# Performance work log

Hardware: AMD Instinct MI355X
Metric: run time of the kernel (lower is better)

## Reference

```python
import jax, jax.numpy as jnp
import numpy as np

N, E = 50000, 800000
IN_DIM, OUT_DIM, EDGE_DIM = 128, 128, 6
LN_EPS = 1e-5


def setup_inputs() -> dict:
    key = jax.random.key(0)
    ks = jax.random.split(key, 9)
    w = lambda k, sh: (jax.random.normal(k, sh, jnp.float32) * 0.05)
    return {
        "x": jax.random.normal(ks[0], (N, IN_DIM), jnp.float32),
        "edge_attr": jax.random.normal(ks[1], (E, EDGE_DIM), jnp.float32),
        "Wn": w(ks[2], (IN_DIM, OUT_DIM)),
        "bn": jnp.zeros((OUT_DIM,), jnp.float32),
        "We": w(ks[3], (EDGE_DIM, OUT_DIM)),
        "be": jnp.zeros((OUT_DIM,), jnp.float32),
        "Wm": w(ks[4], (2 * OUT_DIM, OUT_DIM)),
        "bm": jnp.zeros((OUT_DIM,), jnp.float32),
        "gamma": jnp.ones((OUT_DIM,), jnp.float32),
        "beta": jnp.zeros((OUT_DIM,), jnp.float32),
        "edge_index": jax.random.randint(ks[5], (2, E), 0, N, jnp.int32),
    }


def reference(x, edge_attr, Wn, bn, We, be, Wm, bm, gamma, beta, edge_index):
    row, col = edge_index[0], edge_index[1]
    x_t = x @ Wn + bn                                  # [N, D]
    e_t = edge_attr @ We + be                          # [E, D]
    msgs = jnp.concatenate([x_t[col], e_t], axis=-1)   # gather + concat [E, 2D]
    msgs = jax.nn.relu(msgs @ Wm + bm)                 # [E, D]
    agg = jax.ops.segment_sum(msgs, row, num_segments=N)            # scatter_add
    deg = jax.ops.segment_sum(jnp.ones((E,), jnp.float32), row, num_segments=N)
    out = agg / jnp.clip(deg, 1.0)[:, None] + x_t      # mean-normalize + residual
    mu = out.mean(axis=-1, keepdims=True)
    var = out.var(axis=-1, keepdims=True)
    return (out - mu) * jax.lax.rsqrt(var + LN_EPS) * gamma + beta
```

## Files before the change

kernel.cpp:

```cpp
#include <hip/hip_runtime.h>
#include <hip/hip_bf16.h>

#define D 128
#define EDGE_DIM 6
#define LN_EPS 1e-5f
#define HIST_BLOCKS 2048

typedef __attribute__((ext_vector_type(8))) short short8;
typedef __attribute__((ext_vector_type(4))) float f32x4;
typedef __attribute__((ext_vector_type(2))) float f32x2;

static __device__ __forceinline__ float bf_lo(unsigned u) { return __uint_as_float(u << 16); }
static __device__ __forceinline__ float bf_hi(unsigned u) { return __uint_as_float(u & 0xffff0000u); }
static __device__ __forceinline__ unsigned short f2bf(float f) {
    __hip_bfloat16 h = __float2bfloat16(f);
    return *reinterpret_cast<unsigned short*>(&h);
}

__global__ __launch_bounds__(128)
void setup_all(const float* __restrict__ Wn, const float* __restrict__ bn,
               const float* __restrict__ We, const float* __restrict__ be,
               const float* __restrict__ Wm, const float* __restrict__ bm,
               const int* __restrict__ ei, int E,
               float* __restrict__ Wnm, float* __restrict__ bnm,
               float* __restrict__ Wc, float* __restrict__ bc,
               int* __restrict__ cnt) {
    const int b = blockIdx.x;
    const int d = threadIdx.x;
    if (b < 128) {
        float acc = 0.f;
#pragma unroll 8
        for (int j = 0; j < D; ++j)
            acc = fmaf(Wn[b * D + j], Wm[j * D + d], acc);
        Wnm[b * D + d] = acc;
    } else if (b == 128) {
        float acc = 0.f;
#pragma unroll 8
        for (int j = 0; j < D; ++j)
            acc = fmaf(bn[j], Wm[j * D + d], acc);
        bnm[d] = acc;
    } else if (b < 135) {
        const int k = b - 129;
        float acc = 0.f;
#pragma unroll 8
        for (int j = 0; j < D; ++j)
            acc = fmaf(We[k * D + j], Wm[(D + j) * D + d], acc);
        Wc[k * D + d] = acc;
    } else if (b == 135) {
        float acc = bm[d];
#pragma unroll 8
        for (int j = 0; j < D; ++j)
            acc = fmaf(be[j], Wm[(D + j) * D + d], acc);
        bc[d] = acc;
    } else {
        for (int i = (b - 136) * 128 + d; i < E; i += HIST_BLOCKS * 128)
            atomicAdd(&cnt[ei[i]], 1);
    }
}

__global__ __launch_bounds__(1024)
void scan_pack(const int* __restrict__ cnt, int* __restrict__ start,
               int* __restrict__ cur, int* __restrict__ cursor, int n, int nscan,
               const float* __restrict__ Wn, const float* __restrict__ Wnm,
               unsigned short* __restrict__ Wb) {
    const int tid = threadIdx.x;
    if ((int)blockIdx.x >= nscan) {
        const int idx = ((int)blockIdx.x - nscan) * 1024 + tid;
        if (idx < 4096) {
            const int lane = idx & 63;
            const int s = (idx >> 6) & 3;
            const int ct = (idx >> 8) & 7;
            const int mat = idx >> 11;
            const float* W = mat ? Wnm : Wn;
            const int col = ct * 16 + (lane & 15);
            const int k0 = (lane >> 4) * 8 + 32 * s;
            short8 v;
#pragma unroll
            for (int j = 0; j < 8; ++j)
                v[j] = (short)f2bf(W[(size_t)(k0 + j) * D + col]);
            *reinterpret_cast<short8*>(Wb + (size_t)idx * 8) = v;
        }
        return;
    }
    __shared__ int wsum[16];
    __shared__ int sbase;
    const int lane = tid & 63, wid = tid >> 6;
    const int i = blockIdx.x * 1024 + tid;
    const int v = (i < n) ? cnt[i] : 0;
    int x = v;
#pragma unroll
    for (int off = 1; off < 64; off <<= 1) {
        int t = __shfl_up(x, off);
        if (lane >= off) x += t;
    }
    if (lane == 63) wsum[wid] = x;
    __syncthreads();
    if (wid == 0) {
        int w = (lane < 16) ? wsum[lane] : 0;
#pragma unroll
        for (int off = 1; off < 16; off <<= 1) {
            int t = __shfl_up(w, off);
            if (lane >= off) w += t;
        }
        if (lane < 16) wsum[lane] = w;
    }
    __syncthreads();
    const int total = wsum[15];
    if (tid == 0) sbase = atomicAdd(cursor, total);
    __syncthreads();
    const int woff = (wid > 0) ? wsum[wid - 1] : 0;
    if (i < n) {
        const int sv = sbase + woff + x - v;
        start[i] = sv;
        cur[i] = sv;
    }
}

__global__ __launch_bounds__(256)
void scatter_rec(const int* __restrict__ ei, int E, const float* __restrict__ ea,
                 int* __restrict__ cur, uint4* __restrict__ rec) {
    __shared__ float sEA[256 * EDGE_DIM];
    const int tid = threadIdx.x;
    const int base = blockIdx.x * 256;
    const size_t gbase = (size_t)base * EDGE_DIM;
    const size_t gtot = (size_t)E * EDGE_DIM;
#pragma unroll
    for (int k = 0; k < EDGE_DIM; ++k) {
        const int idx = k * 256 + tid;
        if (gbase + idx < gtot) sEA[idx] = ea[gbase + idx];
    }
    __syncthreads();
    const int e = base + tid;
    if (e < E) {
        const int row = ei[e];
        const int col = ei[E + e];
        const float* ep = &sEA[tid * EDGE_DIM];
        unsigned b01 = (unsigned)f2bf(ep[0]) | ((unsigned)f2bf(ep[1]) << 16);
        unsigned b23 = (unsigned)f2bf(ep[2]) | ((unsigned)f2bf(ep[3]) << 16);
        unsigned b45 = (unsigned)f2bf(ep[4]) | ((unsigned)f2bf(ep[5]) << 16);
        int pos = atomicAdd(&cur[row], 1);
        rec[pos] = make_uint4((unsigned)col, b01, b23, b45);
    }
}

__global__ __launch_bounds__(64)
void gemm_mfma(const float* __restrict__ x, const unsigned short* __restrict__ Wb,
               const float* __restrict__ bn, const float* __restrict__ bnm,
               unsigned short* __restrict__ xtb, unsigned short* __restrict__ hb,
               int nrows) {
    const int lane = threadIdx.x;
    const int row16 = lane & 15;
    const int kgrp = lane >> 4;
    const int t = blockIdx.x;

    float biasA[8], biasB[8];
#pragma unroll
    for (int ct = 0; ct < 8; ++ct) {
        biasA[ct] = bn[ct * 16 + row16];
        biasB[ct] = bnm[ct * 16 + row16];
    }

    const int ra = t * 16 + row16;
    const bool rv = ra < nrows;
    short8 a[4];
#pragma unroll
    for (int s = 0; s < 4; ++s) {
        const float* xp = x + (size_t)ra * D + kgrp * 8 + 32 * s;
        float4 u0 = rv ? *reinterpret_cast<const float4*>(xp)
                       : make_float4(0.f, 0.f, 0.f, 0.f);
        float4 u1 = rv ? *reinterpret_cast<const float4*>(xp + 4)
                       : make_float4(0.f, 0.f, 0.f, 0.f);
        a[s][0] = (short)f2bf(u0.x); a[s][1] = (short)f2bf(u0.y);
        a[s][2] = (short)f2bf(u0.z); a[s][3] = (short)f2bf(u0.w);
        a[s][4] = (short)f2bf(u1.x); a[s][5] = (short)f2bf(u1.y);
        a[s][6] = (short)f2bf(u1.z); a[s][7] = (short)f2bf(u1.w);
    }
    const int rw0 = t * 16 + kgrp * 4;
#pragma unroll
    for (int mat = 0; mat < 2; ++mat) {
        unsigned short* out = mat ? hb : xtb;
#pragma unroll
        for (int ct = 0; ct < 8; ++ct) {
            f32x4 acc = {0.f, 0.f, 0.f, 0.f};
#pragma unroll
            for (int s = 0; s < 4; ++s) {
                short8 bfr = *reinterpret_cast<const short8*>(
                    Wb + (size_t)((((mat * 8 + ct) * 4 + s) * 64 + lane)) * 8);
                acc = __builtin_amdgcn_mfma_f32_16x16x32_bf16(a[s], bfr, acc, 0, 0, 0);
            }
            const float bsc = mat ? biasB[ct] : biasA[ct];
            const int dcol = ct * 16 + row16;
#pragma unroll
            for (int j = 0; j < 4; ++j) {
                const int r = rw0 + j;
                if (r < nrows) out[(size_t)r * D + dcol] = f2bf(acc[j] + bsc);
            }
        }
    }
}

__global__ __launch_bounds__(256)
void aggregate_ln(const unsigned* __restrict__ h,
                  const int* __restrict__ start, const int* __restrict__ cnt,
                  const uint4* __restrict__ rec,
                  const float* __restrict__ Wc, const float* __restrict__ bc,
                  const unsigned* __restrict__ xtb,
                  const float* __restrict__ gamma, const float* __restrict__ beta,
                  float* __restrict__ out, int nnode) {
    const int lane = threadIdx.x & 63;
    const int wid = threadIdx.x >> 6;

    f32x2 wc[EDGE_DIM];
#pragma unroll
    for (int k = 0; k < EDGE_DIM; ++k)
        wc[k] = reinterpret_cast<const f32x2*>(Wc)[k * 64 + lane];
    const f32x2 bc2 = reinterpret_cast<const f32x2*>(bc)[lane];
    const f32x2 g = reinterpret_cast<const f32x2*>(gamma)[lane];
    const f32x2 bb = reinterpret_cast<const f32x2*>(beta)[lane];

    for (int n = blockIdx.x * 4 + wid; n < nnode; n += gridDim.x * 4) {
        const int s = start[n];
        const int c = cnt[n];
        f32x2 axy = {0.f, 0.f};
        for (int ibase = 0; ibase < c; ibase += 64) {
            const int m = min(64, c - ibase);
            uint4 rc = make_uint4(0, 0, 0, 0);
            if (lane < m) rc = rec[(size_t)(s + ibase) + lane];
            auto LDH = [&](int j) -> unsigned {
                const int jc = min(j, m - 1);
                const int colj = __builtin_amdgcn_readlane((int)rc.x, jc);
                return h[(unsigned)(colj * 64 + lane)];
            };
            auto COMP = [&](int j, unsigned hv) {
                const unsigned b01 = (unsigned)__builtin_amdgcn_readlane((int)rc.y, j);
                const unsigned b23 = (unsigned)__builtin_amdgcn_readlane((int)rc.z, j);
                const unsigned b45 = (unsigned)__builtin_amdgcn_readlane((int)rc.w, j);
                f32x2 e01, e23, e45, hx, msg;
                e01[0] = bf_lo(b01); e01[1] = bf_hi(b01);
                e23[0] = bf_lo(b23); e23[1] = bf_hi(b23);
                e45[0] = bf_lo(b45); e45[1] = bf_hi(b45);
                hx[0] = bf_lo(hv); hx[1] = bf_hi(hv);
                asm("v_pk_add_f32 %0, %1, %2" : "=v"(msg) : "v"(bc2), "v"(hx));
                asm("v_pk_fma_f32 %0, %1, %2, %0 op_sel:[0,0,0] op_sel_hi:[0,1,1]"
                    : "+v"(msg) : "s"(e01), "v"(wc[0]));
                asm("v_pk_fma_f32 %0, %1, %2, %0 op_sel:[1,0,0] op_sel_hi:[1,1,1]"
                    : "+v"(msg) : "s"(e01), "v"(wc[1]));
                asm("v_pk_fma_f32 %0, %1, %2, %0 op_sel:[0,0,0] op_sel_hi:[0,1,1]"
                    : "+v"(msg) : "s"(e23), "v"(wc[2]));
                asm("v_pk_fma_f32 %0, %1, %2, %0 op_sel:[1,0,0] op_sel_hi:[1,1,1]"
                    : "+v"(msg) : "s"(e23), "v"(wc[3]));
                asm("v_pk_fma_f32 %0, %1, %2, %0 op_sel:[0,0,0] op_sel_hi:[0,1,1]"
                    : "+v"(msg) : "s"(e45), "v"(wc[4]));
                asm("v_pk_fma_f32 %0, %1, %2, %0 op_sel:[1,0,0] op_sel_hi:[1,1,1]"
                    : "+v"(msg) : "s"(e45), "v"(wc[5]));
                axy[0] += fmaxf(msg[0], 0.f);
                axy[1] += fmaxf(msg[1], 0.f);
            };
            unsigned h0 = LDH(0), h1 = LDH(1), h2 = LDH(2), h3 = LDH(3),
                     h4 = LDH(4), h5 = LDH(5), h6 = LDH(6), h7 = LDH(7);
            int i = 0;
            for (; i + 8 <= m; i += 8) {
                COMP(i + 0, h0); h0 = LDH(i + 8);
                COMP(i + 1, h1); h1 = LDH(i + 9);
                COMP(i + 2, h2); h2 = LDH(i + 10);
                COMP(i + 3, h3); h3 = LDH(i + 11);
                COMP(i + 4, h4); h4 = LDH(i + 12);
                COMP(i + 5, h5); h5 = LDH(i + 13);
                COMP(i + 6, h6); h6 = LDH(i + 14);
                COMP(i + 7, h7); h7 = LDH(i + 15);
            }
            if (i + 0 < m) COMP(i + 0, h0);
            if (i + 1 < m) COMP(i + 1, h1);
            if (i + 2 < m) COMP(i + 2, h2);
            if (i + 3 < m) COMP(i + 3, h3);
            if (i + 4 < m) COMP(i + 4, h4);
            if (i + 5 < m) COMP(i + 5, h5);
            if (i + 6 < m) COMP(i + 6, h6);
        }
        const float inv = 1.0f / fmaxf((float)c, 1.0f);
        const unsigned xu = xtb[(unsigned)(n * 64 + lane)];
        float o0 = fmaf(axy[0], inv, bf_lo(xu));
        float o1 = fmaf(axy[1], inv, bf_hi(xu));
        float s1 = o0 + o1, s2 = o0 * o0 + o1 * o1;
#pragma unroll
        for (int off = 32; off; off >>= 1) {
            s1 += __shfl_xor(s1, off);
            s2 += __shfl_xor(s2, off);
        }
        const float mean = s1 * (1.0f / D);
        const float var = s2 * (1.0f / D) - mean * mean;
        const float rstd = rsqrtf(var + LN_EPS);
        float2 r;
        r.x = (o0 - mean) * rstd * g[0] + bb[0];
        r.y = (o1 - mean) * rstd * g[1] + bb[1];
        reinterpret_cast<float2*>(out)[(size_t)n * 64 + lane] = r;
    }
}

extern "C" void kernel_launch(void* const* d_in, const int* in_sizes, int n_in,
                              void* d_out, int out_size, void* d_ws, size_t ws_size,
                              hipStream_t stream) {
    const float* x     = (const float*)d_in[0];
    const float* eattr = (const float*)d_in[1];
    const float* Wn    = (const float*)d_in[2];
    const float* bn    = (const float*)d_in[3];
    const float* We    = (const float*)d_in[4];
    const float* be    = (const float*)d_in[5];
    const float* Wm    = (const float*)d_in[6];
    const float* bm    = (const float*)d_in[7];
    const float* gamma = (const float*)d_in[8];
    const float* beta  = (const float*)d_in[9];
    const int*   ei    = (const int*)d_in[10];

    const int N = in_sizes[0] / D;
    const int E = in_sizes[10] / 2;

    char* ws = (char*)d_ws;
    unsigned short* xtb = (unsigned short*)ws; ws += (size_t)N * D * 2;
    unsigned short* hb  = (unsigned short*)ws; ws += (size_t)N * D * 2;
    int* ints = (int*)ws;                      ws += (size_t)(N + 4) * 4;
    int* cnt = ints;
    int* cursor = ints + N;
    int* cur    = (int*)ws;                    ws += (size_t)N * 4;
    int* startv = (int*)ws;                    ws += (size_t)N * 4;
    uint4* rec  = (uint4*)ws;                  ws += (size_t)E * 16;
    float* Wnm  = (float*)ws;                  ws += (size_t)D * D * 4;
    float* bnm  = (float*)ws;                  ws += (size_t)D * 4;
    float* Wc   = (float*)ws;                  ws += (size_t)EDGE_DIM * D * 4;
    float* bcv  = (float*)ws;                  ws += (size_t)D * 4;
    unsigned short* Wb = (unsigned short*)ws;  ws += (size_t)4096 * 8 * 2;

    const int nscan = (N + 1023) / 1024;
    const int ntile = (N + 15) / 16;

    hipMemsetAsync(ints, 0, (size_t)(N + 4) * 4, stream);

    setup_all<<<136 + HIST_BLOCKS, 128, 0, stream>>>(Wn, bn, We, be, Wm, bm, ei, E,
                                                     Wnm, bnm, Wc, bcv, cnt);
    scan_pack<<<nscan + 4, 1024, 0, stream>>>(cnt, startv, cur, cursor, N, nscan,
                                              Wn, Wnm, Wb);
    scatter_rec<<<(E + 255) / 256, 256, 0, stream>>>(ei, E, eattr, cur, rec);
    gemm_mfma<<<ntile, 64, 0, stream>>>(x, Wb, bn, bnm, xtb, hb, N);
    aggregate_ln<<<(N + 3) / 4, 256, 0, stream>>>((const unsigned*)hb, startv, cnt, rec,
                                                  Wc, bcv, (const unsigned*)xtb,
                                                  gamma, beta, (float*)d_out, N);
}
```

Baseline: 178.8 us.

## Batch 8 edges per thread in scatter and split FMA chain in aggregate

The scatter kernel now handles 2048 edges per block. It converts edge attributes to packed bf16 in shared memory using float2 loads, then issues 8 independent atomics per thread before writing the records, which exposes more memory-level parallelism. The aggregate kernel splits the dependent pk_fma chain into two accumulators to shorten latency, hoists the residual xtb load ahead of the edge loop, and uses 64-bit pointer arithmetic for the h row address. The risks are fewer blocks (391) for the scatter, higher register use, and one extra add per edge.

```diff
diff --git a/kernel.cpp b/kernel.cpp
--- a/kernel.cpp
+++ b/kernel.cpp
@@ -119,28 +119,34 @@
 __global__ __launch_bounds__(256)
 void scatter_rec(const int* __restrict__ ei, int E, const float* __restrict__ ea,
                  int* __restrict__ cur, uint4* __restrict__ rec) {
-    __shared__ float sEA[256 * EDGE_DIM];
+    __shared__ unsigned sR[2048 * 3];
     const int tid = threadIdx.x;
-    const int base = blockIdx.x * 256;
-    const size_t gbase = (size_t)base * EDGE_DIM;
-    const size_t gtot = (size_t)E * EDGE_DIM;
-#pragma unroll
-    for (int k = 0; k < EDGE_DIM; ++k) {
-        const int idx = k * 256 + tid;
-        if (gbase + idx < gtot) sEA[idx] = ea[gbase + idx];
+    const int base = blockIdx.x * 2048;
+    const int nrec = min(2048, E - base);
+    const float2* ea2 = reinterpret_cast<const float2*>(ea);
+    for (int i = tid; i < nrec * 3; i += 256) {
+        float2 p = ea2[(size_t)base * 3 + i];
+        sR[i] = (unsigned)f2bf(p.x) | ((unsigned)f2bf(p.y) << 16);
     }
     __syncthreads();
-    const int e = base + tid;
-    if (e < E) {
-        const int row = ei[e];
-        const int col = ei[E + e];
-        const float* ep = &sEA[tid * EDGE_DIM];
-        unsigned b01 = (unsigned)f2bf(ep[0]) | ((unsigned)f2bf(ep[1]) << 16);
-        unsigned b23 = (unsigned)f2bf(ep[2]) | ((unsigned)f2bf(ep[3]) << 16);
-        unsigned b45 = (unsigned)f2bf(ep[4]) | ((unsigned)f2bf(ep[5]) << 16);
-        int pos = atomicAdd(&cur[row], 1);
-        rec[pos] = make_uint4((unsigned)col, b01, b23, b45);
-    }
+
+    int rows[8], cols[8], pos[8];
+#pragma unroll
+    for (int it = 0; it < 8; ++it) {
+        const int e = base + it * 256 + tid;
+        const bool val = e < E;
+        rows[it] = val ? ei[e] : -1;
+        cols[it] = val ? ei[E + e] : 0;
+    }
+#pragma unroll
+    for (int it = 0; it < 8; ++it)
+        if (rows[it] >= 0) pos[it] = atomicAdd(&cur[rows[it]], 1);
+#pragma unroll
+    for (int it = 0; it < 8; ++it)
+        if (rows[it] >= 0) {
+            const int le = (it * 256 + tid) * 3;
+            rec[pos[it]] = make_uint4((unsigned)cols[it], sR[le], sR[le + 1], sR[le + 2]);
+        }
 }
 
 __global__ __launch_bounds__(64)
@@ -221,6 +227,7 @@
     for (int n = blockIdx.x * 4 + wid; n < nnode; n += gridDim.x * 4) {
         const int s = start[n];
         const int c = cnt[n];
+        const unsigned xu = xtb[(unsigned)(n * 64 + lane)];
         f32x2 axy = {0.f, 0.f};
         for (int ibase = 0; ibase < c; ibase += 64) {
             const int m = min(64, c - ibase);
@@ -228,33 +235,35 @@
             if (lane < m) rc = rec[(size_t)(s + ibase) + lane];
             auto LDH = [&](int j) -> unsigned {
                 const int jc = min(j, m - 1);
-                const int colj = __builtin_amdgcn_readlane((int)rc.x, jc);
-                return h[(unsigned)(colj * 64 + lane)];
+                const unsigned colj = (unsigned)__builtin_amdgcn_readlane((int)rc.x, jc);
+                const unsigned* hrow = h + ((size_t)colj << 6);
+                return hrow[lane];
             };
             auto COMP = [&](int j, unsigned hv) {
                 const unsigned b01 = (unsigned)__builtin_amdgcn_readlane((int)rc.y, j);
                 const unsigned b23 = (unsigned)__builtin_amdgcn_readlane((int)rc.z, j);
                 const unsigned b45 = (unsigned)__builtin_amdgcn_readlane((int)rc.w, j);
-                f32x2 e01, e23, e45, hx, msg;
+                f32x2 e01, e23, e45, hx, mA, mB;
                 e01[0] = bf_lo(b01); e01[1] = bf_hi(b01);
                 e23[0] = bf_lo(b23); e23[1] = bf_hi(b23);
                 e45[0] = bf_lo(b45); e45[1] = bf_hi(b45);
                 hx[0] = bf_lo(hv); hx[1] = bf_hi(hv);
-                asm("v_pk_add_f32 %0, %1, %2" : "=v"(msg) : "v"(bc2), "v"(hx));
+                asm("v_pk_add_f32 %0, %1, %2" : "=v"(mA) : "v"(bc2), "v"(hx));
+                asm("v_pk_mul_f32 %0, %1, %2 op_sel:[1,0] op_sel_hi:[1,1]"
+                    : "=v"(mB) : "s"(e01), "v"(wc[1]));
                 asm("v_pk_fma_f32 %0, %1, %2, %0 op_sel:[0,0,0] op_sel_hi:[0,1,1]"
-                    : "+v"(msg) : "s"(e01), "v"(wc[0]));
+                    : "+v"(mA) : "s"(e01), "v"(wc[0]));
                 asm("v_pk_fma_f32 %0, %1, %2, %0 op_sel:[1,0,0] op_sel_hi:[1,1,1]"
-                    : "+v"(msg) : "s"(e01), "v"(wc[1]));
+                    : "+v"(mB) : "s"(e23), "v"(wc[3]));
                 asm("v_pk_fma_f32 %0, %1, %2, %0 op_sel:[0,0,0] op_sel_hi:[0,1,1]"
-                    : "+v"(msg) : "s"(e23), "v"(wc[2]));
+                    : "+v"(mA) : "s"(e23), "v"(wc[2]));
                 asm("v_pk_fma_f32 %0, %1, %2, %0 op_sel:[1,0,0] op_sel_hi:[1,1,1]"
-                    : "+v"(msg) : "s"(e23), "v"(wc[3]));
+                    : "+v"(mB) : "s"(e45), "v"(wc[5]));
                 asm("v_pk_fma_f32 %0, %1, %2, %0 op_sel:[0,0,0] op_sel_hi:[0,1,1]"
-                    : "+v"(msg) : "s"(e45), "v"(wc[4]));
-                asm("v_pk_fma_f32 %0, %1, %2, %0 op_sel:[1,0,0] op_sel_hi:[1,1,1]"
-                    : "+v"(msg) : "s"(e45), "v"(wc[5]));
-                axy[0] += fmaxf(msg[0], 0.f);
-                axy[1] += fmaxf(msg[1], 0.f);
+                    : "+v"(mA) : "s"(e45), "v"(wc[4]));
+                asm("v_pk_add_f32 %0, %0, %1" : "+v"(mA) : "v"(mB));
+                axy[0] += fmaxf(mA[0], 0.f);
+                axy[1] += fmaxf(mA[1], 0.f);
             };
             unsigned h0 = LDH(0), h1 = LDH(1), h2 = LDH(2), h3 = LDH(3),
                      h4 = LDH(4), h5 = LDH(5), h6 = LDH(6), h7 = LDH(7);
@@ -278,7 +287,6 @@
             if (i + 6 < m) COMP(i + 6, h6);
         }
         const float inv = 1.0f / fmaxf((float)c, 1.0f);
-        const unsigned xu = xtb[(unsigned)(n * 64 + lane)];
         float o0 = fmaf(axy[0], inv, bf_lo(xu));
         float o1 = fmaf(axy[1], inv, bf_hi(xu));
         float s1 = o0 + o1, s2 = o0 * o0 + o1 * o1;
@@ -339,7 +347,7 @@
                                                      Wnm, bnm, Wc, bcv, cnt);
     scan_pack<<<nscan + 4, 1024, 0, stream>>>(cnt, startv, cur, cursor, N, nscan,
                                               Wn, Wnm, Wb);
-    scatter_rec<<<(E + 255) / 256, 256, 0, stream>>>(ei, E, eattr, cur, rec);
+    scatter_rec<<<(E + 2047) / 2048, 256, 0, stream>>>(ei, E, eattr, cur, rec);
     gemm_mfma<<<ntile, 64, 0, stream>>>(x, Wb, bn, bnm, xtb, hb, N);
     aggregate_ln<<<(N + 3) / 4, 256, 0, stream>>>((const unsigned*)hb, startv, cnt, rec,
                                                   Wc, bcv, (const unsigned*)xtb,
```

After: 173.2 us. -3.1%, faster.
